# Optimization experiments

Hardware: AMD Instinct MI355X
Metric: run time of the kernel (lower is better)

The kernel has to match this reference:

```python
import jax, jax.numpy as jnp
import numpy as np

B, D_IN, EXPERT_DIM, N_EXPERT, N_TASK = 16384, 1024, 256, 8, 4


def setup_inputs() -> dict:
    key = jax.random.key(0)
    k1, k2, k3 = jax.random.split(key, 3)
    x = jax.random.normal(k1, (B, D_IN), dtype=jnp.float32)
    # Glorot-ish scaling for weights
    We = jax.random.normal(k2, (N_EXPERT, D_IN, EXPERT_DIM), dtype=jnp.float32) * (1.0 / np.sqrt(D_IN))
    be = jnp.zeros((N_EXPERT, EXPERT_DIM), dtype=jnp.float32)
    Wg = jax.random.normal(k3, (N_TASK, D_IN, N_EXPERT), dtype=jnp.float32) * (1.0 / np.sqrt(D_IN))
    bg = jnp.zeros((N_TASK, N_EXPERT), dtype=jnp.float32)
    return {"x": x, "We": We, "be": be, "Wg": Wg, "bg": bg}


def reference(x, We, be, Wg, bg):
    # Experts: grouped GEMM -> [B, n_expert, expert_dim]
    E = jax.nn.relu(jnp.einsum("bd,edh->beh", x, We) + be[None, :, :])
    # Gates: [B, n_task, n_expert], softmax over experts
    G = jax.nn.softmax(jnp.einsum("bd,tde->bte", x, Wg) + bg[None, :, :], axis=-1)
    # Gated combine per task: towers[t] = E^T @ g_t -> [n_task, B, expert_dim]
    towers = jnp.einsum("beh,bte->tbh", E, G)
    return towers  # stacked version of the original list of [B, expert_dim] towers
```

## Files before the change

kernel.cpp:

```cpp
#include <hip/hip_runtime.h>

#define B_ROWS 16384
#define D_IN   1024
#define H_DIM  256
#define N_EXP  8
#define N_TASK 4
#define NKT    16

typedef short bf16x8 __attribute__((ext_vector_type(8)));
typedef float f32x4  __attribute__((ext_vector_type(4)));
typedef unsigned short u16x8 __attribute__((ext_vector_type(8)));

static __device__ __forceinline__ unsigned short f2bf(float f) {
  unsigned int u = __float_as_uint(f);
  u += 0x7fffu + ((u >> 16) & 1u);
  return (unsigned short)(u >> 16);
}

#define WS_XB   0u
#define WS_WET  33554432u
#define WS_GT   37814272u

__global__ __launch_bounds__(256) void k_prep_gates(const float* __restrict__ x,
                                                    const float* __restrict__ We,
                                                    const float* __restrict__ Wg,
                                                    unsigned short* __restrict__ x_b,
                                                    unsigned short* __restrict__ We_t,
                                                    const float* __restrict__ bg,
                                                    float* __restrict__ Gt) {
  __shared__ char smem[75264];
  int bid = blockIdx.x;
  int t = threadIdx.x;

  if (bid < 512) {
    unsigned short (*tile)[72] = (unsigned short (*)[72])smem;
    int e = bid >> 6;
    int tl = bid & 63;
    int k0 = (tl >> 2) * 64, h0 = (tl & 3) * 64;
    const float* src = We + (size_t)e * (D_IN * H_DIM);
#pragma unroll
    for (int i = 0; i < 4; ++i) {
      int kk = (t >> 4) + i * 16;
      int hh = (t & 15) * 4;
      float4 v = *(const float4*)(src + (size_t)(k0 + kk) * H_DIM + h0 + hh);
      tile[hh + 0][kk] = f2bf(v.x);
      tile[hh + 1][kk] = f2bf(v.y);
      tile[hh + 2][kk] = f2bf(v.z);
      tile[hh + 3][kk] = f2bf(v.w);
    }
    __syncthreads();
    unsigned short* dst = We_t + (size_t)e * (H_DIM * D_IN);
#pragma unroll
    for (int i = 0; i < 4; ++i) {
      int hh = (t >> 4) + i * 16;
      int kk = (t & 15) * 4;
      ushort4 u = *(const ushort4*)&tile[hh][kk];
      *(ushort4*)(dst + (size_t)(h0 + hh) * D_IN + k0 + kk) = u;
    }
    return;
  }

  unsigned short* wgs = (unsigned short*)smem;
  float (*red)[16][36] = (float (*)[16][36])(smem + 66048);
  int m0 = (bid - 512) * 16;

#pragma unroll
  for (int i = 0; i < 32; ++i) {
    int idx = t * 4 + i * 1024;
    float4 v = *(const float4*)(Wg + idx);
    int kk = (idx >> 3) & 1023;
    int nb = ((idx >> 13) << 3) + (idx & 7);
    wgs[(size_t)(nb + 0) * 1032 + kk] = f2bf(v.x);
    wgs[(size_t)(nb + 1) * 1032 + kk] = f2bf(v.y);
    wgs[(size_t)(nb + 2) * 1032 + kk] = f2bf(v.z);
    wgs[(size_t)(nb + 3) * 1032 + kk] = f2bf(v.w);
  }
  __syncthreads();

  int w = t >> 6, l = t & 63;
  int lr = l & 15, lq = l >> 4;
  int kbase = w * 256;
  f32x4 acc0 = {0.f, 0.f, 0.f, 0.f}, acc1 = {0.f, 0.f, 0.f, 0.f};

  const float* xrow = x + (size_t)(m0 + lr) * D_IN;
  unsigned short* xbrow = x_b + (size_t)(m0 + lr) * D_IN;
  const unsigned short* wg0 = wgs + (size_t)lr * 1032;
  const unsigned short* wg1 = wgs + (size_t)(16 + lr) * 1032;

#pragma unroll
  for (int ks = 0; ks < 8; ++ks) {
    int k = kbase + ks * 32 + lq * 8;
    float4 v0 = *(const float4*)(xrow + k);
    float4 v1 = *(const float4*)(xrow + k + 4);
    bf16x8 a;
    a[0] = (short)f2bf(v0.x); a[1] = (short)f2bf(v0.y);
    a[2] = (short)f2bf(v0.z); a[3] = (short)f2bf(v0.w);
    a[4] = (short)f2bf(v1.x); a[5] = (short)f2bf(v1.y);
    a[6] = (short)f2bf(v1.z); a[7] = (short)f2bf(v1.w);
    *(bf16x8*)(xbrow + k) = a;
    bf16x8 b0 = *(const bf16x8*)(wg0 + k);
    bf16x8 b1 = *(const bf16x8*)(wg1 + k);
    acc0 = __builtin_amdgcn_mfma_f32_16x16x32_bf16(a, b0, acc0, 0, 0, 0);
    acc1 = __builtin_amdgcn_mfma_f32_16x16x32_bf16(a, b1, acc1, 0, 0, 0);
  }

#pragma unroll
  for (int j = 0; j < 4; ++j) {
    red[w][lq * 4 + j][lr]      = acc0[j];
    red[w][lq * 4 + j][16 + lr] = acc1[j];
  }
  __syncthreads();
  if (w == 0) {
#pragma unroll
    for (int j = 0; j < 4; ++j) {
      int rr = lq * 4 + j;
      acc0[j] = red[0][rr][lr] + red[1][rr][lr] + red[2][rr][lr] + red[3][rr][lr];
      acc1[j] = red[0][rr][16 + lr] + red[1][rr][16 + lr] + red[2][rr][16 + lr] + red[3][rr][16 + lr];
    }
    int colb = lr;
    int rbase = m0 + lq * 4;
    float bga = bg[colb], bgb = bg[16 + colb];
#pragma unroll
    for (int j = 0; j < 4; ++j) {
      float va = acc0[j] + bga;
      float vb = acc1[j] + bgb;
      float mxa = va, mxb = vb;
#pragma unroll
      for (int d = 1; d < 8; d <<= 1) {
        mxa = fmaxf(mxa, __shfl_xor(mxa, d));
        mxb = fmaxf(mxb, __shfl_xor(mxb, d));
      }
      va = __expf(va - mxa); vb = __expf(vb - mxb);
      float sa = va, sb = vb;
#pragma unroll
      for (int d = 1; d < 8; d <<= 1) {
        sa += __shfl_xor(sa, d);
        sb += __shfl_xor(sb, d);
      }
      va /= sa; vb /= sb;
      Gt[(size_t)colb * B_ROWS + rbase + j]        = va;
      Gt[(size_t)(16 + colb) * B_ROWS + rbase + j] = vb;
    }
  }
}

__global__ __launch_bounds__(512, 2) void k_expert(const unsigned short* __restrict__ x_b,
                                                   const unsigned short* __restrict__ We_t,
                                                   const float* __restrict__ be,
                                                   const float* __restrict__ Gt,
                                                   float* __restrict__ out) {
  __shared__ unsigned short As[2][256 * 64];
  __shared__ unsigned short Bs[2][256 * 64];
  int bid = blockIdx.x;
  int t = threadIdx.x;

  int xcd = bid & 7;
  int idx = bid >> 3;
  int m   = xcd * 8 + (idx >> 3);
  int hs  = idx & 7;
  int m0  = m * 256;

  int w  = t >> 6, l = t & 63;
  int wm = w >> 2, wn = w & 3;
  int lr = l & 15, lq = l >> 4;

  const unsigned short* Ab = x_b + (size_t)m0 * D_IN;

  const int sr = t >> 3, sg = t & 7;
  const int swz0 = ((lq ^ (lr & 7)) << 3);
  const int swz1 = (((4 + lq) ^ (lr & 7)) << 3);
  const int arow0 = (wm * 128 + lr) << 6;
  const int brow0 = (wn * 64 + lr) << 6;

  size_t bsrc[4];
#pragma unroll
  for (int q2 = 0; q2 < 4; ++q2) {
    int rq = q2 * 64 + sr;
    int me = (rq >> 3) & 7;
    int mh = hs * 32 + ((rq >> 6) & 3) * 8 + (rq & 7);
    bsrc[q2] = (size_t)(me * H_DIM + mh) * D_IN + (size_t)((sg ^ (rq & 7)) << 3);
  }

  f32x4 acc[8][4];
#pragma unroll
  for (int i = 0; i < 8; ++i)
#pragma unroll
    for (int j = 0; j < 4; ++j) acc[i][j] = (f32x4){0.f, 0.f, 0.f, 0.f};

#define STAGE_A(cb, kt, h)                                                                       \
  do {                                                                                           \
    int r0_ = (h) * 128 + sr;                                                                    \
    int r1_ = r0_ + 64;                                                                          \
    __builtin_amdgcn_global_load_lds(                                                            \
        (const __attribute__((address_space(1))) void*)(Ab + (size_t)r0_ * D_IN + (kt) * 64 +    \
                                                        ((sg ^ (r0_ & 7)) << 3)),                \
        (__attribute__((address_space(3))) void*)(&As[(cb)][r0_ * 64 + sg * 8]), 16, 0, 0);      \
    __builtin_amdgcn_global_load_lds(                                                            \
        (const __attribute__((address_space(1))) void*)(Ab + (size_t)r1_ * D_IN + (kt) * 64 +    \
                                                        ((sg ^ (r1_ & 7)) << 3)),                \
        (__attribute__((address_space(3))) void*)(&As[(cb)][r1_ * 64 + sg * 8]), 16, 0, 0);      \
  } while (0)
#define STAGE_B(cb, kt, h)                                                                       \
  do {                                                                                           \
    int r0_ = (h) * 128 + sr;                                                                    \
    int r1_ = r0_ + 64;                                                                          \
    __builtin_amdgcn_global_load_lds(                                                            \
        (const __attribute__((address_space(1))) void*)(We_t + bsrc[2 * (h)] + (kt) * 64),       \
        (__attribute__((address_space(3))) void*)(&Bs[(cb)][r0_ * 64 + sg * 8]), 16, 0, 0);      \
    __builtin_amdgcn_global_load_lds(                                                            \
        (const __attribute__((address_space(1))) void*)(We_t + bsrc[2 * (h) + 1] + (kt) * 64),   \
        (__attribute__((address_space(3))) void*)(&Bs[(cb)][r1_ * 64 + sg * 8]), 16, 0, 0);      \
  } while (0)

  STAGE_A(0, 0, 0); STAGE_A(0, 0, 1);
  STAGE_B(0, 0, 0); STAGE_B(0, 0, 1);
  STAGE_B(1, 1, 0); STAGE_B(1, 1, 1);
  asm volatile("s_waitcnt vmcnt(4)" ::: "memory");
  __builtin_amdgcn_s_barrier();

#pragma unroll 2
  for (int kt = 0; kt < NKT; ++kt) {
    int c = kt & 1;
    const unsigned short* Ap = &As[c][0];
    const unsigned short* Bp = &Bs[c][0];
    bf16x8 b0[4], b1[4];
#pragma unroll
    for (int q = 0; q < 4; ++q) {
      if (q == 0) {
#pragma unroll
        for (int fn = 0; fn < 4; ++fn) {
          b0[fn] = *(const bf16x8*)(Bp + brow0 + fn * 1024 + swz0);
          b1[fn] = *(const bf16x8*)(Bp + brow0 + fn * 1024 + swz1);
        }
      }
      bf16x8 a00 = *(const bf16x8*)(Ap + arow0 + (2 * q) * 1024 + swz0);
      bf16x8 a01 = *(const bf16x8*)(Ap + arow0 + (2 * q) * 1024 + swz1);
      bf16x8 a10 = *(const bf16x8*)(Ap + arow0 + (2 * q + 1) * 1024 + swz0);
      bf16x8 a11 = *(const bf16x8*)(Ap + arow0 + (2 * q + 1) * 1024 + swz1);
      if (q == 0)      { if (kt + 1 < NKT) STAGE_A(c ^ 1, kt + 1, 0); }
      else if (q == 1) { if (kt + 1 < NKT) STAGE_A(c ^ 1, kt + 1, 1); }
      else if (q == 2) { if (kt + 2 < NKT) STAGE_B(c, kt + 2, 0); }
      else             { if (kt + 2 < NKT) STAGE_B(c, kt + 2, 1); }
      __builtin_amdgcn_s_barrier();
      asm volatile("s_waitcnt lgkmcnt(0)" ::: "memory");
      __builtin_amdgcn_s_setprio(1);
#pragma unroll
      for (int fn = 0; fn < 4; ++fn) {
        acc[2 * q][fn]     = __builtin_amdgcn_mfma_f32_16x16x32_bf16(a00, b0[fn], acc[2 * q][fn], 0, 0, 0);
        acc[2 * q][fn]     = __builtin_amdgcn_mfma_f32_16x16x32_bf16(a01, b1[fn], acc[2 * q][fn], 0, 0, 0);
        acc[2 * q + 1][fn] = __builtin_amdgcn_mfma_f32_16x16x32_bf16(a10, b0[fn], acc[2 * q + 1][fn], 0, 0, 0);
        acc[2 * q + 1][fn] = __builtin_amdgcn_mfma_f32_16x16x32_bf16(a11, b1[fn], acc[2 * q + 1][fn], 0, 0, 0);
      }
      __builtin_amdgcn_s_setprio(0);
      if (q == 3) {
        if (kt < NKT - 2)        asm volatile("s_waitcnt vmcnt(4)" ::: "memory");
        else if (kt == NKT - 2)  asm volatile("s_waitcnt vmcnt(0)" ::: "memory");
      }
      __builtin_amdgcn_s_barrier();
    }
  }
#undef STAGE_A
#undef STAGE_B

  float (*Gl)[260] = (float (*)[260])(&As[0][0]);
  {
    int n  = t >> 4;
    int c0 = (t & 15) * 16;
    const float* gsrc = Gt + (size_t)n * B_ROWS + m0 + c0;
    f32x4 g0 = *(const f32x4*)(gsrc + 0);
    f32x4 g1 = *(const f32x4*)(gsrc + 4);
    f32x4 g2 = *(const f32x4*)(gsrc + 8);
    f32x4 g3 = *(const f32x4*)(gsrc + 12);
    *(f32x4*)&Gl[n][c0 + 0]  = g0;
    *(f32x4*)&Gl[n][c0 + 4]  = g1;
    *(f32x4*)&Gl[n][c0 + 8]  = g2;
    *(f32x4*)&Gl[n][c0 + 12] = g3;
  }
  __syncthreads();

  int hi = lr >> 3, h7 = lr & 7;
  int hglob = hs * 32 + wn * 8 + h7;
  float bev[4];
#pragma unroll
  for (int fn = 0; fn < 4; ++fn)
    bev[fn] = be[(2 * fn + hi) * H_DIM + hglob];
#pragma unroll
  for (int fm = 0; fm < 8; ++fm) {
    int rloc = wm * 128 + fm * 16 + lq * 4;
    int r0 = m0 + rloc;
    float vv[4][4];
#pragma unroll
    for (int fn = 0; fn < 4; ++fn)
#pragma unroll
      for (int j = 0; j < 4; ++j)
        vv[fn][j] = fmaxf(acc[fm][fn][j] + bev[fn], 0.f);
    float p[4][4];
#pragma unroll
    for (int tk = 0; tk < 4; ++tk) {
      f32x4 gv[4];
#pragma unroll
      for (int fn = 0; fn < 4; ++fn)
        gv[fn] = *(const f32x4*)&Gl[tk * 8 + 2 * fn + hi][rloc];
#pragma unroll
      for (int j = 0; j < 4; ++j)
        p[tk][j] = gv[0][j] * vv[0][j] + gv[1][j] * vv[1][j] +
                   gv[2][j] * vv[2][j] + gv[3][j] * vv[3][j];
    }
#pragma unroll
    for (int j = 0; j < 4; ++j) {
      float sa = hi ? p[0][j] : p[2][j];
      float sb = hi ? p[1][j] : p[3][j];
      float ra = __shfl_xor(sa, 8);
      float rb = __shfl_xor(sb, 8);
      float t0 = (hi ? p[2][j] : p[0][j]) + ra;
      float t1 = (hi ? p[3][j] : p[1][j]) + rb;
      size_t tk0 = (size_t)(hi * 2);
      out[(tk0 * B_ROWS + r0 + j) * H_DIM + hglob]       = t0;
      out[((tk0 + 1) * B_ROWS + r0 + j) * H_DIM + hglob] = t1;
    }
  }
}

extern "C" void kernel_launch(void* const* d_in, const int* in_sizes, int n_in,
                              void* d_out, int out_size, void* d_ws, size_t ws_size,
                              hipStream_t stream) {
  const float* x  = (const float*)d_in[0];
  const float* We = (const float*)d_in[1];
  const float* be = (const float*)d_in[2];
  const float* Wg = (const float*)d_in[3];
  const float* bg = (const float*)d_in[4];
  float* out = (float*)d_out;
  char* ws = (char*)d_ws;
  unsigned short* x_b  = (unsigned short*)(ws + WS_XB);
  unsigned short* We_t = (unsigned short*)(ws + WS_WET);
  float*          Gt   = (float*)(ws + WS_GT);

  k_prep_gates<<<1536, 256, 0, stream>>>(x, We, Wg, x_b, We_t, bg, Gt);
  k_expert<<<512, 512, 0, stream>>>(x_b, We_t, be, Gt, out);
}
```

Baseline: 199.1 us.

## Rework gate prep with 512-thread blocks and FP32 scalar gate dot products

The prep kernel now uses 512-thread blocks, handling two We transpose tiles per block and 32 gate rows per block. This halves how often each block stages Wg into shared memory. Gate logits are now computed with FP32 FMAs on bf16-loaded weights, reduced across 16 lanes by shuffles, instead of MFMA plus a shared-memory reduction. The expert kernel's gate-tile load is remapped and padded to 264 to change its shared-memory bank pattern. The scalar FMA loop has 32 accumulators per thread and a heavy shuffle reduction, which may raise register pressure and ALU cost.

```diff
diff --git a/kernel.cpp b/kernel.cpp
--- a/kernel.cpp
+++ b/kernel.cpp
@@ -16,32 +16,37 @@
   u += 0x7fffu + ((u >> 16) & 1u);
   return (unsigned short)(u >> 16);
 }
+static __device__ __forceinline__ float bf2f(unsigned short u) {
+  return __uint_as_float(((unsigned int)u) << 16);
+}
 
 #define WS_XB   0u
 #define WS_WET  33554432u
 #define WS_GT   37814272u
 
-__global__ __launch_bounds__(256) void k_prep_gates(const float* __restrict__ x,
+__global__ __launch_bounds__(512) void k_prep_gates(const float* __restrict__ x,
                                                     const float* __restrict__ We,
                                                     const float* __restrict__ Wg,
                                                     unsigned short* __restrict__ x_b,
                                                     unsigned short* __restrict__ We_t,
                                                     const float* __restrict__ bg,
                                                     float* __restrict__ Gt) {
-  __shared__ char smem[75264];
+  __shared__ char smem[66048];
   int bid = blockIdx.x;
   int t = threadIdx.x;
 
-  if (bid < 512) {
-    unsigned short (*tile)[72] = (unsigned short (*)[72])smem;
-    int e = bid >> 6;
-    int tl = bid & 63;
+  if (bid < 256) {
+    unsigned short (*tile)[72] = (unsigned short (*)[72])(smem + (t >> 8) * 9216);
+    int tl2 = bid * 2 + (t >> 8);
+    int e = tl2 >> 6;
+    int tl = tl2 & 63;
     int k0 = (tl >> 2) * 64, h0 = (tl & 3) * 64;
+    int tt = t & 255;
     const float* src = We + (size_t)e * (D_IN * H_DIM);
 #pragma unroll
     for (int i = 0; i < 4; ++i) {
-      int kk = (t >> 4) + i * 16;
-      int hh = (t & 15) * 4;
+      int kk = (tt >> 4) + i * 16;
+      int hh = (tt & 15) * 4;
       float4 v = *(const float4*)(src + (size_t)(k0 + kk) * H_DIM + h0 + hh);
       tile[hh + 0][kk] = f2bf(v.x);
       tile[hh + 1][kk] = f2bf(v.y);
@@ -52,8 +57,8 @@
     unsigned short* dst = We_t + (size_t)e * (H_DIM * D_IN);
 #pragma unroll
     for (int i = 0; i < 4; ++i) {
-      int hh = (t >> 4) + i * 16;
-      int kk = (t & 15) * 4;
+      int hh = (tt >> 4) + i * 16;
+      int kk = (tt & 15) * 4;
       ushort4 u = *(const ushort4*)&tile[hh][kk];
       *(ushort4*)(dst + (size_t)(h0 + hh) * D_IN + k0 + kk) = u;
     }
@@ -61,15 +66,14 @@
   }
 
   unsigned short* wgs = (unsigned short*)smem;
-  float (*red)[16][36] = (float (*)[16][36])(smem + 66048);
-  int m0 = (bid - 512) * 16;
-
-#pragma unroll
-  for (int i = 0; i < 32; ++i) {
-    int idx = t * 4 + i * 1024;
+  int m0 = (bid - 256) * 32;
+
+#pragma unroll 4
+  for (int i = 0; i < 16; ++i) {
+    int idx = t * 4 + i * 2048;
     float4 v = *(const float4*)(Wg + idx);
     int kk = (idx >> 3) & 1023;
-    int nb = ((idx >> 13) << 3) + (idx & 7);
+    int nb = (idx >> 13) * 8 + (idx & 7);
     wgs[(size_t)(nb + 0) * 1032 + kk] = f2bf(v.x);
     wgs[(size_t)(nb + 1) * 1032 + kk] = f2bf(v.y);
     wgs[(size_t)(nb + 2) * 1032 + kk] = f2bf(v.z);
@@ -77,70 +81,60 @@
   }
   __syncthreads();
 
-  int w = t >> 6, l = t & 63;
-  int lr = l & 15, lq = l >> 4;
-  int kbase = w * 256;
-  f32x4 acc0 = {0.f, 0.f, 0.f, 0.f}, acc1 = {0.f, 0.f, 0.f, 0.f};
-
-  const float* xrow = x + (size_t)(m0 + lr) * D_IN;
-  unsigned short* xbrow = x_b + (size_t)(m0 + lr) * D_IN;
-  const unsigned short* wg0 = wgs + (size_t)lr * 1032;
-  const unsigned short* wg1 = wgs + (size_t)(16 + lr) * 1032;
-
-#pragma unroll
-  for (int ks = 0; ks < 8; ++ks) {
-    int k = kbase + ks * 32 + lq * 8;
-    float4 v0 = *(const float4*)(xrow + k);
-    float4 v1 = *(const float4*)(xrow + k + 4);
+  int r = t >> 4, s = t & 15;
+  const float* xrow = x + (size_t)(m0 + r) * D_IN;
+  unsigned short* xbrow = x_b + (size_t)(m0 + r) * D_IN;
+
+  float acc[32];
+#pragma unroll
+  for (int n = 0; n < 32; ++n) acc[n] = 0.f;
+
+#pragma unroll 2
+  for (int i = 0; i < 8; ++i) {
+    int k0 = i * 128 + s * 8;
+    float4 v0 = *(const float4*)(xrow + k0);
+    float4 v1 = *(const float4*)(xrow + k0 + 4);
+    float xf[8] = {v0.x, v0.y, v0.z, v0.w, v1.x, v1.y, v1.z, v1.w};
     bf16x8 a;
-    a[0] = (short)f2bf(v0.x); a[1] = (short)f2bf(v0.y);
-    a[2] = (short)f2bf(v0.z); a[3] = (short)f2bf(v0.w);
-    a[4] = (short)f2bf(v1.x); a[5] = (short)f2bf(v1.y);
-    a[6] = (short)f2bf(v1.z); a[7] = (short)f2bf(v1.w);
-    *(bf16x8*)(xbrow + k) = a;
-    bf16x8 b0 = *(const bf16x8*)(wg0 + k);
-    bf16x8 b1 = *(const bf16x8*)(wg1 + k);
-    acc0 = __builtin_amdgcn_mfma_f32_16x16x32_bf16(a, b0, acc0, 0, 0, 0);
-    acc1 = __builtin_amdgcn_mfma_f32_16x16x32_bf16(a, b1, acc1, 0, 0, 0);
-  }
-
-#pragma unroll
-  for (int j = 0; j < 4; ++j) {
-    red[w][lq * 4 + j][lr]      = acc0[j];
-    red[w][lq * 4 + j][16 + lr] = acc1[j];
-  }
-  __syncthreads();
-  if (w == 0) {
-#pragma unroll
-    for (int j = 0; j < 4; ++j) {
-      int rr = lq * 4 + j;
-      acc0[j] = red[0][rr][lr] + red[1][rr][lr] + red[2][rr][lr] + red[3][rr][lr];
-      acc1[j] = red[0][rr][16 + lr] + red[1][rr][16 + lr] + red[2][rr][16 + lr] + red[3][rr][16 + lr];
-    }
-    int colb = lr;
-    int rbase = m0 + lq * 4;
-    float bga = bg[colb], bgb = bg[16 + colb];
-#pragma unroll
-    for (int j = 0; j < 4; ++j) {
-      float va = acc0[j] + bga;
-      float vb = acc1[j] + bgb;
-      float mxa = va, mxb = vb;
-#pragma unroll
-      for (int d = 1; d < 8; d <<= 1) {
-        mxa = fmaxf(mxa, __shfl_xor(mxa, d));
-        mxb = fmaxf(mxb, __shfl_xor(mxb, d));
-      }
-      va = __expf(va - mxa); vb = __expf(vb - mxb);
-      float sa = va, sb = vb;
-#pragma unroll
-      for (int d = 1; d < 8; d <<= 1) {
-        sa += __shfl_xor(sa, d);
-        sb += __shfl_xor(sb, d);
-      }
-      va /= sa; vb /= sb;
-      Gt[(size_t)colb * B_ROWS + rbase + j]        = va;
-      Gt[(size_t)(16 + colb) * B_ROWS + rbase + j] = vb;
-    }
+#pragma unroll
+    for (int j = 0; j < 8; ++j) a[j] = (short)f2bf(xf[j]);
+    *(bf16x8*)(xbrow + k0) = a;
+#pragma unroll
+    for (int n = 0; n < 32; ++n) {
+      u16x8 wv = *(const u16x8*)&wgs[(size_t)n * 1032 + k0];
+#pragma unroll
+      for (int j = 0; j < 8; ++j)
+        acc[n] += xf[j] * bf2f((unsigned short)wv[j]);
+    }
+  }
+
+#pragma unroll
+  for (int d = 1; d < 16; d <<= 1)
+#pragma unroll
+    for (int n = 0; n < 32; ++n) acc[n] += __shfl_xor(acc[n], d);
+
+#pragma unroll
+  for (int c = 0; c < 8; ++c) {
+    float4 b = *(const float4*)(bg + c * 4);
+    acc[c * 4 + 0] += b.x; acc[c * 4 + 1] += b.y;
+    acc[c * 4 + 2] += b.z; acc[c * 4 + 3] += b.w;
+  }
+#pragma unroll
+  for (int tk = 0; tk < 4; ++tk) {
+    float mx = acc[tk * 8];
+#pragma unroll
+    for (int e = 1; e < 8; ++e) mx = fmaxf(mx, acc[tk * 8 + e]);
+    float ssum = 0.f;
+#pragma unroll
+    for (int e = 0; e < 8; ++e) { acc[tk * 8 + e] = __expf(acc[tk * 8 + e] - mx); ssum += acc[tk * 8 + e]; }
+    float inv = 1.f / ssum;
+#pragma unroll
+    for (int e = 0; e < 8; ++e) acc[tk * 8 + e] *= inv;
+  }
+  if (s == 0) {
+#pragma unroll
+    for (int n = 0; n < 32; ++n)
+      Gt[(size_t)n * B_ROWS + m0 + r] = acc[n];
   }
 }
 
@@ -262,10 +256,10 @@
 #undef STAGE_A
 #undef STAGE_B
 
-  float (*Gl)[260] = (float (*)[260])(&As[0][0]);
+  float (*Gl)[264] = (float (*)[264])(&As[0][0]);
   {
-    int n  = t >> 4;
-    int c0 = (t & 15) * 16;
+    int n  = t & 31;
+    int c0 = (t >> 5) * 16;
     const float* gsrc = Gt + (size_t)n * B_ROWS + m0 + c0;
     f32x4 g0 = *(const f32x4*)(gsrc + 0);
     f32x4 g1 = *(const f32x4*)(gsrc + 4);
@@ -335,6 +329,6 @@
   unsigned short* We_t = (unsigned short*)(ws + WS_WET);
   float*          Gt   = (float*)(ws + WS_GT);
 
-  k_prep_gates<<<1536, 256, 0, stream>>>(x, We, Wg, x_b, We_t, bg, Gt);
+  k_prep_gates<<<768, 512, 0, stream>>>(x, We, Wg, x_b, We_t, bg, Gt);
   k_expert<<<512, 512, 0, stream>>>(x_b, We_t, be, Gt, out);
 }
```

Measured after the change: 223.3 us. +12.1%, slower.
